# Performance work log

Hardware: AMD Instinct MI355X
Metric: run time of the kernel (lower is better)

The kernel has to match this reference:

```python
import jax, jax.numpy as jnp
import numpy as np

B, S, HID = 1, 2048, 4096
N_HEADS, N_KV, HEAD_DIM = 32, 8, 128
N_REP = N_HEADS // N_KV
ROPE_THETA = 10000.0
NEG_INF = -1e9


def setup_inputs() -> dict:
    key = jax.random.key(0)
    ks = jax.random.split(key, 5)
    hidden_states = jax.random.normal(ks[0], (B, S, HID), dtype=jnp.float32)
    Wq = jax.random.normal(ks[1], (HID, N_HEADS * HEAD_DIM), dtype=jnp.float32) * 0.02
    Wk = jax.random.normal(ks[2], (HID, N_KV * HEAD_DIM), dtype=jnp.float32) * 0.02
    Wv = jax.random.normal(ks[3], (HID, N_KV * HEAD_DIM), dtype=jnp.float32) * 0.02
    Wo = jax.random.normal(ks[4], (N_HEADS * HEAD_DIM, HID), dtype=jnp.float32) * 0.02
    # causal additive mask [B, 1, S, S]
    causal = jnp.tril(jnp.ones((S, S), dtype=bool))
    attention_mask = jnp.where(causal, 0.0, NEG_INF).astype(jnp.float32)[None, None]
    position_ids = jnp.broadcast_to(jnp.arange(S, dtype=jnp.int32)[None], (B, S))
    return {
        "hidden_states": hidden_states, "Wq": Wq, "Wk": Wk, "Wv": Wv, "Wo": Wo,
        "attention_mask": attention_mask, "position_ids": position_ids,
    }


def _rotate_half(x):
    half = x.shape[-1] // 2
    return jnp.concatenate([-x[..., half:], x[..., :half]], axis=-1)


def _rope_tables(position_ids):
    # inv_freq: [head_dim/2]
    inv_freq = 1.0 / (ROPE_THETA ** (jnp.arange(0, HEAD_DIM, 2, dtype=jnp.float32) / HEAD_DIM))
    # freqs: [B, S, head_dim/2]
    freqs = position_ids.astype(jnp.float32)[..., None] * inv_freq
    emb = jnp.concatenate([freqs, freqs], axis=-1)  # [B, S, head_dim]
    # [B, 1, S, head_dim] to broadcast over heads
    return jnp.cos(emb)[:, None], jnp.sin(emb)[:, None]


def reference(hidden_states, Wq, Wk, Wv, Wo, attention_mask, position_ids):
    b, s, _ = hidden_states.shape
    # projections -> [B, H, S, D]
    q = (hidden_states @ Wq).reshape(b, s, N_HEADS, HEAD_DIM).transpose(0, 2, 1, 3)
    k = (hidden_states @ Wk).reshape(b, s, N_KV, HEAD_DIM).transpose(0, 2, 1, 3)
    v = (hidden_states @ Wv).reshape(b, s, N_KV, HEAD_DIM).transpose(0, 2, 1, 3)
    cos, sin = _rope_tables(position_ids)
    q = q * cos + _rotate_half(q) * sin
    k = k * cos + _rotate_half(k) * sin
    # GQA repeat_kv (repeat_interleave over head dim)
    k = jnp.repeat(k, N_REP, axis=1)
    v = jnp.repeat(v, N_REP, axis=1)
    scores = jnp.einsum("bhqd,bhkd->bhqk", q, k) / jnp.sqrt(jnp.float32(HEAD_DIM))
    scores = scores + attention_mask
    probs = jax.nn.softmax(scores.astype(jnp.float32), axis=-1).astype(q.dtype)
    attn = jnp.einsum("bhqk,bhkd->bhqd", probs, v)
    attn = attn.transpose(0, 2, 1, 3).reshape(b, s, N_HEADS * HEAD_DIM)
    return attn @ Wo
```

## Files before the change

kernel.cpp:

```cpp
#include <hip/hip_runtime.h>
#include <hip/hip_bf16.h>
#include <math.h>

#define S_LEN 2048
#define HIDDEN 4096
#define NH 32
#define NKV 8
#define HD 128
#define NQKV 6144

typedef __bf16 bf16_t;
typedef __bf16 bf16x8 __attribute__((ext_vector_type(8)));
typedef __bf16 bf16x4 __attribute__((ext_vector_type(4)));
typedef float f32x4 __attribute__((ext_vector_type(4)));

typedef __attribute__((address_space(1))) void gvoid;
typedef __attribute__((address_space(3))) void lvoid;

__device__ __forceinline__ void gload_lds16(const void* g, void* l) {
    __builtin_amdgcn_global_load_lds((gvoid*)g, (lvoid*)l, 16, 0, 0);
}

__global__ void cast_bf16_kernel(const float* __restrict__ in, bf16_t* __restrict__ out, int n4) {
    int stride = gridDim.x * blockDim.x;
    for (int idx = blockIdx.x * blockDim.x + threadIdx.x; idx < n4; idx += stride) {
        float4 v = ((const float4*)in)[idx];
        bf16x4 o;
        o.x = (bf16_t)v.x; o.y = (bf16_t)v.y; o.z = (bf16_t)v.z; o.w = (bf16_t)v.w;
        ((bf16x4*)out)[idx] = o;
    }
}

__global__ __launch_bounds__(256) void transpose_cast_kernel(const float* __restrict__ in,
                                                             bf16_t* __restrict__ out,
                                                             int ldin, int ldout) {
    __shared__ float t[32][33];
    int c0 = blockIdx.x * 32, r0 = blockIdx.y * 32;
    int tx = threadIdx.x, ty = threadIdx.y;
#pragma unroll
    for (int i = 0; i < 4; ++i)
        t[ty + i * 8][tx] = in[(size_t)(r0 + ty + i * 8) * ldin + c0 + tx];
    __syncthreads();
#pragma unroll
    for (int i = 0; i < 4; ++i)
        out[(size_t)(c0 + ty + i * 8) * ldout + r0 + tx] = (bf16_t)t[tx][ty + i * 8];
}

__global__ __launch_bounds__(512, 2) void gemm_ring_kernel(const bf16_t* __restrict__ A,
                                                           const bf16_t* __restrict__ Bt,
                                                           float* __restrict__ C,
                                                           int M, int N, int K) {
    __shared__ bf16_t As[3][128 * 32];
    __shared__ bf16_t Bs[3][256 * 32];
    const int tid = threadIdx.x;
    const int lane = tid & 63, w = tid >> 6;
    const int wm = w >> 2, wn = w & 3;
    const int g = lane >> 4, c16 = lane & 15;
    const int srow = lane >> 2;
    const int scg = ((lane & 3) ^ ((lane >> 3) & 3)) * 8;
    const int rdc = (g ^ ((c16 >> 1) & 3)) * 8;

    const int nbm = M / 128;
    const int cpx = gridDim.x >> 3;
    const int bid = blockIdx.x;
    const int swz = (bid & 7) * cpx + (bid >> 3);
    const int bm = swz % nbm, bn = swz / nbm;

    const bf16_t* Ab = A + (size_t)(bm * 128) * K;
    const bf16_t* Bb = Bt + (size_t)(bn * 256) * K;

    auto stage = [&](int slot, int kt) {
        const bf16_t* Ak = Ab + (size_t)kt * 32;
        const bf16_t* Bk = Bb + (size_t)kt * 32;
        {
            int rb = 16 * w;
            gload_lds16(Ak + (size_t)(rb + srow) * K + scg, &As[slot][rb * 32]);
        }
#pragma unroll
        for (int j = 0; j < 2; ++j) {
            int rb = 32 * w + 16 * j;
            gload_lds16(Bk + (size_t)(rb + srow) * K + scg, &Bs[slot][rb * 32]);
        }
    };

    f32x4 acc[4][4];
#pragma unroll
    for (int i = 0; i < 4; ++i)
#pragma unroll
        for (int j = 0; j < 4; ++j)
            acc[i][j] = (f32x4){0.f, 0.f, 0.f, 0.f};

    const int NT = K / 32;
    stage(0, 0);
    stage(1, 1);

    int slot = 0, slot2 = 2;
    for (int t = 0; t < NT; ++t) {
        asm volatile("s_waitcnt vmcnt(3)" ::: "memory");
        __builtin_amdgcn_s_barrier();
        __builtin_amdgcn_sched_barrier(0);

        bf16x8 af[4], bf[4];
#pragma unroll
        for (int i = 0; i < 4; ++i) {
            int arow = wm * 64 + i * 16 + c16;
            af[i] = *(const bf16x8*)&As[slot][arow * 32 + rdc];
            int brow = wn * 64 + i * 16 + c16;
            bf[i] = *(const bf16x8*)&Bs[slot][brow * 32 + rdc];
        }
        int nk = t + 2;
        if (nk >= NT) nk -= NT;
        stage(slot2, nk);

        asm volatile("s_waitcnt lgkmcnt(0)" ::: "memory");
        __builtin_amdgcn_sched_barrier(0);
        __builtin_amdgcn_s_setprio(1);
#pragma unroll
        for (int i = 0; i < 4; ++i)
#pragma unroll
            for (int j = 0; j < 4; ++j)
                acc[i][j] = __builtin_amdgcn_mfma_f32_16x16x32_bf16(af[i], bf[j], acc[i][j], 0, 0, 0);
        __builtin_amdgcn_s_setprio(0);

        slot = slot2;
        slot = (slot + 2) % 3;
        slot2 = (slot + 2) % 3;
    }

#pragma unroll
    for (int mi = 0; mi < 4; ++mi)
#pragma unroll
        for (int ni = 0; ni < 4; ++ni) {
            int col = bn * 256 + wn * 64 + ni * 16 + c16;
#pragma unroll
            for (int r = 0; r < 4; ++r) {
                int row = bm * 128 + wm * 64 + mi * 16 + g * 4 + r;
                C[(size_t)row * N + col] = acc[mi][ni][r];
            }
        }
}

__global__ void rope_kernel(const float* __restrict__ in, bf16_t* __restrict__ out,
                            const int* __restrict__ pos, int H, int ld, float scale) {
    int idx = blockIdx.x * blockDim.x + threadIdx.x;
    int total = S_LEN * H * 64;
    if (idx >= total) return;
    int d = idx & 63;
    int h = (idx >> 6) % H;
    int s = idx / (64 * H);
    const float* base = in + (size_t)s * ld + h * HD;
    float x0 = base[d], x1 = base[d + 64];
    float p = (float)pos[s];
    float invf = __expf(-0.14391156831212787f * (float)d);
    float f = p * invf;
    float sn, cs;
    __sincosf(f, &sn, &cs);
    float o0 = (x0 * cs - x1 * sn) * scale;
    float o1 = (x1 * cs + x0 * sn) * scale;
    bf16_t* ob = out + ((size_t)h * S_LEN + s) * HD;
    ob[d] = (bf16_t)o0;
    ob[d + 64] = (bf16_t)o1;
}

#define PLD 72
__global__ __launch_bounds__(256) void attn_kernel(const bf16_t* __restrict__ Q,
                                                   const bf16_t* __restrict__ K,
                                                   const bf16_t* __restrict__ Vt,
                                                   bf16_t* __restrict__ O) {
    __shared__ bf16_t Ks[2][64 * 128];
    __shared__ bf16_t Vs[2][128 * 64];
    __shared__ bf16_t Pl[4][16 * PLD];
    const int tid = threadIdx.x;
    const int lane = tid & 63, w = tid >> 6;
    const int bid = blockIdx.x;
    const int h = bid & 31;
    const int x = bid >> 5;
    const int kv = h >> 2;
    const int qb = x * 64 + w * 16;
    const int g = lane >> 4, c16 = lane & 15;
    const int c7 = c16 & 7;
    const bf16_t* Qh = Q + (size_t)h * S_LEN * HD;
    const bf16_t* Kh = K + (size_t)kv * S_LEN * HD;
    const bf16_t* Vh = Vt + (size_t)kv * HD * S_LEN;
    bf16_t* P = Pl[w];

    auto stage = [&](int buf, int kb) {
        bf16_t* Kd = Ks[buf];
        bf16_t* Vd = Vs[buf];
#pragma unroll
        for (int j = 0; j < 4; ++j) {
            int i = w * 4 + j;
            {
                int row = 4 * i + (lane >> 4);
                int sc = (lane & 15) ^ (row & 7);
                gload_lds16(Kh + (size_t)(kb + row) * HD + sc * 8, Kd + i * 512);
            }
            {
                int row = 8 * i + (lane >> 3);
                int sc = (lane & 7) ^ ((lane >> 3) & 7);
                gload_lds16(Vh + (size_t)row * S_LEN + kb + sc * 8, Vd + i * 512);
            }
        }
    };

    bf16x8 qf[4];
#pragma unroll
    for (int c = 0; c < 4; ++c)
        qf[c] = *(const bf16x8*)(Qh + (size_t)(qb + c16) * HD + c * 32 + g * 8);

    f32x4 acc_o[8];
#pragma unroll
    for (int dt = 0; dt < 8; ++dt) acc_o[dt] = (f32x4){0.f, 0.f, 0.f, 0.f};
    float m[4] = {-1e30f, -1e30f, -1e30f, -1e30f};
    float l[4] = {0.f, 0.f, 0.f, 0.f};

    const int nkt = x + 1;
    stage(0, 0);
    __syncthreads();
    int cur = 0;

    for (int kt = 0; kt < nkt; ++kt) {
        if (kt + 1 < nkt) stage(cur ^ 1, (kt + 1) * 64);
        const int kb = kt * 64;
        const bf16_t* Kb = Ks[cur];
        const bf16_t* Vb = Vs[cur];
        const bool diag = (kt == nkt - 1);

        f32x4 sacc[4];
#pragma unroll
        for (int t = 0; t < 4; ++t) sacc[t] = (f32x4){0.f, 0.f, 0.f, 0.f};
#pragma unroll
        for (int t = 0; t < 4; ++t) {
            const bf16_t* krow = Kb + (t * 16 + c16) * 128;
#pragma unroll
            for (int cc = 0; cc < 4; ++cc) {
                bf16x8 kf = *(const bf16x8*)(krow + (((cc * 4 + g) ^ c7) * 8));
                sacc[t] = __builtin_amdgcn_mfma_f32_16x16x32_bf16(qf[cc], kf, sacc[t], 0, 0, 0);
            }
        }
        float p[4][4], alpha[4];
#pragma unroll
        for (int r = 0; r < 4; ++r) {
            int qq = qb + g * 4 + r;
            float s[4];
#pragma unroll
            for (int t = 0; t < 4; ++t)
                s[t] = (!diag || (kb + t * 16 + c16 <= qq)) ? sacc[t][r] : -1e30f;
            float mx = fmaxf(fmaxf(s[0], s[1]), fmaxf(s[2], s[3]));
            mx = fmaxf(mx, __shfl_xor(mx, 1));
            mx = fmaxf(mx, __shfl_xor(mx, 2));
            mx = fmaxf(mx, __shfl_xor(mx, 4));
            mx = fmaxf(mx, __shfl_xor(mx, 8));
            float mn = fmaxf(m[r], mx);
            alpha[r] = __expf(m[r] - mn);
            m[r] = mn;
            float rs = 0.f;
#pragma unroll
            for (int t = 0; t < 4; ++t) {
                p[t][r] = __expf(s[t] - mn);
                rs += p[t][r];
            }
            rs += __shfl_xor(rs, 1);
            rs += __shfl_xor(rs, 2);
            rs += __shfl_xor(rs, 4);
            rs += __shfl_xor(rs, 8);
            l[r] = l[r] * alpha[r] + rs;
        }
#pragma unroll
        for (int dt = 0; dt < 8; ++dt)
#pragma unroll
            for (int r = 0; r < 4; ++r) acc_o[dt][r] *= alpha[r];
#pragma unroll
        for (int t = 0; t < 4; ++t)
#pragma unroll
            for (int r = 0; r < 4; ++r)
                P[(g * 4 + r) * PLD + t * 16 + c16] = (bf16_t)p[t][r];
        bf16x8 pf[2];
        pf[0] = *(const bf16x8*)(P + c16 * PLD + g * 8);
        pf[1] = *(const bf16x8*)(P + c16 * PLD + 32 + g * 8);
#pragma unroll
        for (int dt = 0; dt < 8; ++dt) {
            const bf16_t* vrow = Vb + (dt * 16 + c16) * 64;
            bf16x8 vf0 = *(const bf16x8*)(vrow + ((g ^ c7) * 8));
            bf16x8 vf1 = *(const bf16x8*)(vrow + (((4 + g) ^ c7) * 8));
            acc_o[dt] = __builtin_amdgcn_mfma_f32_16x16x32_bf16(pf[0], vf0, acc_o[dt], 0, 0, 0);
            acc_o[dt] = __builtin_amdgcn_mfma_f32_16x16x32_bf16(pf[1], vf1, acc_o[dt], 0, 0, 0);
        }
        __syncthreads();
        cur ^= 1;
    }
    float inv_l[4];
#pragma unroll
    for (int r = 0; r < 4; ++r) inv_l[r] = 1.f / l[r];
#pragma unroll
    for (int dt = 0; dt < 8; ++dt)
#pragma unroll
        for (int r = 0; r < 4; ++r)
            O[(size_t)(qb + g * 4 + r) * HIDDEN + h * HD + dt * 16 + c16] =
                (bf16_t)(acc_o[dt][r] * inv_l[r]);
}

extern "C" void kernel_launch(void* const* d_in, const int* in_sizes, int n_in,
                              void* d_out, int out_size, void* d_ws, size_t ws_size,
                              hipStream_t stream) {
    const float* hs = (const float*)d_in[0];
    const float* Wq = (const float*)d_in[1];
    const float* Wk = (const float*)d_in[2];
    const float* Wv = (const float*)d_in[3];
    const float* Wo = (const float*)d_in[4];
    const int* pos = (const int*)d_in[6];
    float* out = (float*)d_out;

    char* ws = (char*)d_ws;
    size_t off = 0;
    auto alloc = [&](size_t bytes) -> void* {
        void* p = ws + off;
        off += (bytes + 255) & ~(size_t)255;
        return p;
    };
    bf16_t* hB    = (bf16_t*)alloc((size_t)S_LEN * HIDDEN * 2);
    bf16_t* WqkvT = (bf16_t*)alloc((size_t)NQKV * HIDDEN * 2);
    bf16_t* WoT   = (bf16_t*)alloc((size_t)HIDDEN * HIDDEN * 2);
    float*  QKV   = (float*)alloc((size_t)S_LEN * NQKV * 4);
    bf16_t* Qr    = (bf16_t*)alloc((size_t)NH * S_LEN * HD * 2);
    bf16_t* Kr    = (bf16_t*)alloc((size_t)NKV * S_LEN * HD * 2);
    bf16_t* Vt    = (bf16_t*)alloc((size_t)NKV * HD * S_LEN * 2);
    bf16_t* Oat   = (bf16_t*)alloc((size_t)S_LEN * HIDDEN * 2);

    dim3 tb(32, 8);
    cast_bf16_kernel<<<2048, 256, 0, stream>>>(hs, hB, S_LEN * HIDDEN / 4);
    transpose_cast_kernel<<<dim3(HIDDEN / 32, HIDDEN / 32), tb, 0, stream>>>(Wq, WqkvT, HIDDEN, HIDDEN);
    transpose_cast_kernel<<<dim3(1024 / 32, HIDDEN / 32), tb, 0, stream>>>(Wk, WqkvT + (size_t)4096 * HIDDEN, 1024, HIDDEN);
    transpose_cast_kernel<<<dim3(1024 / 32, HIDDEN / 32), tb, 0, stream>>>(Wv, WqkvT + (size_t)5120 * HIDDEN, 1024, HIDDEN);
    transpose_cast_kernel<<<dim3(HIDDEN / 32, HIDDEN / 32), tb, 0, stream>>>(Wo, WoT, HIDDEN, HIDDEN);
    gemm_ring_kernel<<<(S_LEN / 128) * (NQKV / 256), 512, 0, stream>>>(hB, WqkvT, QKV, S_LEN, NQKV, HIDDEN);
    rope_kernel<<<(S_LEN * NH * 64 + 255) / 256, 256, 0, stream>>>(QKV, Qr, pos, NH, NQKV, 0.08838834764831843f);
    rope_kernel<<<(S_LEN * NKV * 64 + 255) / 256, 256, 0, stream>>>(QKV + 4096, Kr, pos, NKV, NQKV, 1.0f);
    transpose_cast_kernel<<<dim3(1024 / 32, S_LEN / 32), tb, 0, stream>>>(QKV + 5120, Vt, NQKV, S_LEN);
    attn_kernel<<<1024, 256, 0, stream>>>(Qr, Kr, Vt, Oat);
    gemm_ring_kernel<<<(S_LEN / 128) * (HIDDEN / 256), 512, 0, stream>>>(Oat, WoT, out, S_LEN, HIDDEN, HIDDEN);
}
```

Measured before the change: 389.0 us.

## Store QKV in bf16, use exp2 softmax with folded log2e, tweak GEMM scheduling

The QKV projection GEMM now writes bf16 instead of fp32. This halves the intermediate buffer traffic for the rope and V-transpose kernels, which are adapted to read bf16. The attention softmax switches from __expf to the native exp2 instruction, with log2(e) folded into the Q scale, and the rope inverse-frequency also uses exp2. The GEMM drops the explicit lgkmcnt wait and sched barrier before the MFMAs, raises priority earlier, and simplifies the ring slot arithmetic. Rounding QKV to bf16 before rope adds a small precision loss. Removing the explicit LDS wait relies on the compiler to insert the correct waits.

```diff
diff --git a/kernel.cpp b/kernel.cpp
--- a/kernel.cpp
+++ b/kernel.cpp
@@ -1,6 +1,5 @@
 #include <hip/hip_runtime.h>
 #include <hip/hip_bf16.h>
-#include <math.h>
 
 #define S_LEN 2048
 #define HIDDEN 4096
@@ -19,6 +18,10 @@
 
 __device__ __forceinline__ void gload_lds16(const void* g, void* l) {
     __builtin_amdgcn_global_load_lds((gvoid*)g, (lvoid*)l, 16, 0, 0);
+}
+
+__device__ __forceinline__ float fast_exp2(float x) {
+    return __builtin_amdgcn_exp2f(x);
 }
 
 __global__ void cast_bf16_kernel(const float* __restrict__ in, bf16_t* __restrict__ out, int n4) {
@@ -46,9 +49,25 @@
         out[(size_t)(c0 + ty + i * 8) * ldout + r0 + tx] = (bf16_t)t[tx][ty + i * 8];
 }
 
+__global__ __launch_bounds__(256) void transpose_bf16_kernel(const bf16_t* __restrict__ in,
+                                                             bf16_t* __restrict__ out,
+                                                             int ldin, int ldout) {
+    __shared__ float t[32][33];
+    int c0 = blockIdx.x * 32, r0 = blockIdx.y * 32;
+    int tx = threadIdx.x, ty = threadIdx.y;
+#pragma unroll
+    for (int i = 0; i < 4; ++i)
+        t[ty + i * 8][tx] = (float)in[(size_t)(r0 + ty + i * 8) * ldin + c0 + tx];
+    __syncthreads();
+#pragma unroll
+    for (int i = 0; i < 4; ++i)
+        out[(size_t)(c0 + ty + i * 8) * ldout + r0 + tx] = (bf16_t)t[tx][ty + i * 8];
+}
+
+template<typename OutT>
 __global__ __launch_bounds__(512, 2) void gemm_ring_kernel(const bf16_t* __restrict__ A,
                                                            const bf16_t* __restrict__ Bt,
-                                                           float* __restrict__ C,
+                                                           OutT* __restrict__ C,
                                                            int M, int N, int K) {
     __shared__ bf16_t As[3][128 * 32];
     __shared__ bf16_t Bs[3][256 * 32];
@@ -99,6 +118,7 @@
         asm volatile("s_waitcnt vmcnt(3)" ::: "memory");
         __builtin_amdgcn_s_barrier();
         __builtin_amdgcn_sched_barrier(0);
+        __builtin_amdgcn_s_setprio(1);
 
         bf16x8 af[4], bf[4];
 #pragma unroll
@@ -112,9 +132,6 @@
         if (nk >= NT) nk -= NT;
         stage(slot2, nk);
 
-        asm volatile("s_waitcnt lgkmcnt(0)" ::: "memory");
-        __builtin_amdgcn_sched_barrier(0);
-        __builtin_amdgcn_s_setprio(1);
 #pragma unroll
         for (int i = 0; i < 4; ++i)
 #pragma unroll
@@ -122,9 +139,8 @@
                 acc[i][j] = __builtin_amdgcn_mfma_f32_16x16x32_bf16(af[i], bf[j], acc[i][j], 0, 0, 0);
         __builtin_amdgcn_s_setprio(0);
 
-        slot = slot2;
-        slot = (slot + 2) % 3;
-        slot2 = (slot + 2) % 3;
+        slot = (slot + 1) % 3;
+        slot2 = (slot2 + 1) % 3;
     }
 
 #pragma unroll
@@ -135,12 +151,12 @@
 #pragma unroll
             for (int r = 0; r < 4; ++r) {
                 int row = bm * 128 + wm * 64 + mi * 16 + g * 4 + r;
-                C[(size_t)row * N + col] = acc[mi][ni][r];
-            }
-        }
-}
-
-__global__ void rope_kernel(const float* __restrict__ in, bf16_t* __restrict__ out,
+                C[(size_t)row * N + col] = (OutT)acc[mi][ni][r];
+            }
+        }
+}
+
+__global__ void rope_kernel(const bf16_t* __restrict__ in, bf16_t* __restrict__ out,
                             const int* __restrict__ pos, int H, int ld, float scale) {
     int idx = blockIdx.x * blockDim.x + threadIdx.x;
     int total = S_LEN * H * 64;
@@ -148,10 +164,10 @@
     int d = idx & 63;
     int h = (idx >> 6) % H;
     int s = idx / (64 * H);
-    const float* base = in + (size_t)s * ld + h * HD;
-    float x0 = base[d], x1 = base[d + 64];
+    const bf16_t* base = in + (size_t)s * ld + h * HD;
+    float x0 = (float)base[d], x1 = (float)base[d + 64];
     float p = (float)pos[s];
-    float invf = __expf(-0.14391156831212787f * (float)d);
+    float invf = fast_exp2(-0.20762050593046935f * (float)d);
     float f = p * invf;
     float sn, cs;
     __sincosf(f, &sn, &cs);
@@ -252,12 +268,12 @@
             mx = fmaxf(mx, __shfl_xor(mx, 4));
             mx = fmaxf(mx, __shfl_xor(mx, 8));
             float mn = fmaxf(m[r], mx);
-            alpha[r] = __expf(m[r] - mn);
+            alpha[r] = fast_exp2(m[r] - mn);
             m[r] = mn;
             float rs = 0.f;
 #pragma unroll
             for (int t = 0; t < 4; ++t) {
-                p[t][r] = __expf(s[t] - mn);
+                p[t][r] = fast_exp2(s[t] - mn);
                 rs += p[t][r];
             }
             rs += __shfl_xor(rs, 1);
@@ -321,7 +337,7 @@
     bf16_t* hB    = (bf16_t*)alloc((size_t)S_LEN * HIDDEN * 2);
     bf16_t* WqkvT = (bf16_t*)alloc((size_t)NQKV * HIDDEN * 2);
     bf16_t* WoT   = (bf16_t*)alloc((size_t)HIDDEN * HIDDEN * 2);
-    float*  QKV   = (float*)alloc((size_t)S_LEN * NQKV * 4);
+    bf16_t* QKV   = (bf16_t*)alloc((size_t)S_LEN * NQKV * 2);
     bf16_t* Qr    = (bf16_t*)alloc((size_t)NH * S_LEN * HD * 2);
     bf16_t* Kr    = (bf16_t*)alloc((size_t)NKV * S_LEN * HD * 2);
     bf16_t* Vt    = (bf16_t*)alloc((size_t)NKV * HD * S_LEN * 2);
@@ -333,10 +349,10 @@
     transpose_cast_kernel<<<dim3(1024 / 32, HIDDEN / 32), tb, 0, stream>>>(Wk, WqkvT + (size_t)4096 * HIDDEN, 1024, HIDDEN);
     transpose_cast_kernel<<<dim3(1024 / 32, HIDDEN / 32), tb, 0, stream>>>(Wv, WqkvT + (size_t)5120 * HIDDEN, 1024, HIDDEN);
     transpose_cast_kernel<<<dim3(HIDDEN / 32, HIDDEN / 32), tb, 0, stream>>>(Wo, WoT, HIDDEN, HIDDEN);
-    gemm_ring_kernel<<<(S_LEN / 128) * (NQKV / 256), 512, 0, stream>>>(hB, WqkvT, QKV, S_LEN, NQKV, HIDDEN);
-    rope_kernel<<<(S_LEN * NH * 64 + 255) / 256, 256, 0, stream>>>(QKV, Qr, pos, NH, NQKV, 0.08838834764831843f);
+    gemm_ring_kernel<bf16_t><<<(S_LEN / 128) * (NQKV / 256), 512, 0, stream>>>(hB, WqkvT, QKV, S_LEN, NQKV, HIDDEN);
+    rope_kernel<<<(S_LEN * NH * 64 + 255) / 256, 256, 0, stream>>>(QKV, Qr, pos, NH, NQKV, 0.1275174310f);
     rope_kernel<<<(S_LEN * NKV * 64 + 255) / 256, 256, 0, stream>>>(QKV + 4096, Kr, pos, NKV, NQKV, 1.0f);
-    transpose_cast_kernel<<<dim3(1024 / 32, S_LEN / 32), tb, 0, stream>>>(QKV + 5120, Vt, NQKV, S_LEN);
+    transpose_bf16_kernel<<<dim3(1024 / 32, S_LEN / 32), tb, 0, stream>>>(QKV + 5120, Vt, NQKV, S_LEN);
     attn_kernel<<<1024, 256, 0, stream>>>(Qr, Kr, Vt, Oat);
-    gemm_ring_kernel<<<(S_LEN / 128) * (HIDDEN / 256), 512, 0, stream>>>(Oat, WoT, out, S_LEN, HIDDEN, HIDDEN);
-}
+    gemm_ring_kernel<float><<<(S_LEN / 128) * (HIDDEN / 256), 512, 0, stream>>>(Oat, WoT, out, S_LEN, HIDDEN, HIDDEN);
+}
```

Result: no change. 384.6 us (-1.1%).
